# Performance work log

Hardware: AMD Instinct MI355X
Metric: run time of the kernel (lower is better)

The kernel has to match this reference:

```python
import jax, jax.numpy as jnp
import numpy as np

EPS = 1e-12

def l2norm(x, axis):
    # torch.nn.functional.normalize: x / max(||x||_2, eps)
    n = jnp.sqrt(jnp.sum(x * x, axis=axis, keepdims=True))
    return x / jnp.maximum(n, EPS)

def setup_inputs() -> dict:
    key = jax.random.key(0)
    k1, k2, k3, k4 = jax.random.split(key, 4)
    B, Cf, H, W = 128, 1024, 16, 16
    n_att, dv = 312, 300
    img = jax.random.normal(k1, (B, Cf, H, W), dtype=jnp.float32)
    # V is initialized from row-normalized w2v embeddings in the module
    V = l2norm(jax.random.normal(k2, (n_att, dv), dtype=jnp.float32), axis=1)
    W1 = jax.random.normal(k3, (dv, Cf), dtype=jnp.float32)
    W2 = jax.random.normal(k4, (dv, Cf), dtype=jnp.float32)
    return {"img": img, "V": V, "W1": W1, "W2": W2}

def reference(img, V, W1, W2):
    vv = l2norm(V, axis=1)                               # [i, v]
    B, Cf, H, Wd = img.shape
    av = l2norm(img.reshape(B, Cf, H * Wd), axis=1)      # [b, f, r]
    Q = vv @ W1                                          # [i, f]
    A = jnp.einsum('if,bfr->bir', Q, av)                 # attention logits
    A = jax.nn.softmax(A, axis=-1)
    F_p = jnp.einsum('bir,bfr->bif', A, av)              # attended features
    Pred_att = jnp.einsum('if,bif->bi', vv @ W2, F_p)
    return Pred_att
```

## Files before the change

kernel.cpp:

```cpp
#include <hip/hip_runtime.h>
#include <math.h>

#define NB   128
#define CF   1024
#define RR   256
#define NA   312
#define DV   300
#define M2   320
#define MT   640
#define NKC  32

typedef _Float16 half8  __attribute__((ext_vector_type(8)));
typedef float float16v  __attribute__((ext_vector_type(16)));

__device__ __forceinline__ void gload16(const void* g, void* l) {
    __builtin_amdgcn_global_load_lds(
        (const __attribute__((address_space(1))) void*)g,
        (__attribute__((address_space(3))) void*)l, 16, 0, 0);
}

__global__ void k_prep(const float* __restrict__ img, float* __restrict__ sumsq,
                       _Float16* __restrict__ avT) {
    int fs = blockIdx.x, rc = blockIdx.y, b = blockIdx.z;
    int r0 = rc * 64;
    int t = threadIdx.x;
    __shared__ __align__(16) char sm[64 * 65 * 4];
    _Float16 (*tile)[65] = (_Float16 (*)[65])sm;
    float    (*ssb)[65]  = (float    (*)[65])sm;
    int fl = t >> 2, cg = t & 3;
    int rl = t >> 2, g  = t & 3;
    float ss[16];
    #pragma unroll
    for (int j = 0; j < 16; ++j) ss[j] = 0.f;

    for (int fc = 0; fc < 4; ++fc) {
        int f0 = fs * 256 + fc * 64;
        const float4* p4 = (const float4*)(img + ((size_t)(b * CF + f0 + fl)) * RR + r0 + cg * 16);
        float4 v0 = p4[0], v1 = p4[1], v2 = p4[2], v3 = p4[3];
        __syncthreads();
        float xs[16] = {v0.x, v0.y, v0.z, v0.w, v1.x, v1.y, v1.z, v1.w,
                        v2.x, v2.y, v2.z, v2.w, v3.x, v3.y, v3.z, v3.w};
        #pragma unroll
        for (int j = 0; j < 16; ++j) {
            ss[j] += xs[j] * xs[j];
            tile[fl][cg * 16 + j] = (_Float16)xs[j];
        }
        __syncthreads();
        int kc  = (f0 >> 5) + (g >> 1);
        int kkb = (g & 1) * 16;
        half8 o0, o1;
        #pragma unroll
        for (int j = 0; j < 8; ++j) o0[j] = tile[g * 16 + j][rl];
        #pragma unroll
        for (int j = 0; j < 8; ++j) o1[j] = tile[g * 16 + 8 + j][rl];
        _Float16* q = avT + (((size_t)(b * NKC + kc) * RR + r0 + rl) * 32 + kkb);
        *(half8*)q       = o0;
        *(half8*)(q + 8) = o1;
    }
    __syncthreads();
    #pragma unroll
    for (int j = 0; j < 16; ++j) ssb[fl][cg * 16 + j] = ss[j];
    __syncthreads();
    if (t < 64) {
        float tot = 0.f;
        for (int f2 = 0; f2 < 64; ++f2) tot += ssb[f2][t];
        atomicAdd(&sumsq[b * RR + r0 + t], tot);
    }
}

__global__ void k_q(const float* __restrict__ V, const float* __restrict__ W1,
                    const float* __restrict__ W2, _Float16* __restrict__ Qb) {
    int ib = blockIdx.x;
    int f  = blockIdx.y * 256 + threadIdx.x;
    int i0 = ib * 8;
    int t  = threadIdx.x;
    __shared__ float inv8[8];
    float acc[8] = {0,0,0,0,0,0,0,0};
    bool zero = (ib == 39 || ib == 79);
    int v0 = (ib < 40) ? i0 : i0 - M2;
    if (!zero) {
        int row = t >> 5, l32 = t & 31;
        float s = 0.f;
        for (int v = l32; v < DV; v += 32) { float x = V[(v0 + row) * DV + v]; s += x * x; }
        #pragma unroll
        for (int o = 16; o; o >>= 1) s += __shfl_xor(s, o, 32);
        if (l32 == 0) inv8[row] = 1.f / fmaxf(sqrtf(s), 1e-12f);
        __syncthreads();
        const float* W = (ib < 40) ? W1 : W2;
        for (int v = 0; v < DV; ++v) {
            float wv = W[(size_t)v * CF + f];
            #pragma unroll
            for (int ii = 0; ii < 8; ++ii) acc[ii] += V[(v0 + ii) * DV + v] * wv;
        }
        #pragma unroll
        for (int ii = 0; ii < 8; ++ii) acc[ii] *= inv8[ii];
    }
    #pragma unroll
    for (int ii = 0; ii < 8; ++ii)
        Qb[((size_t)(f >> 5) * MT + (i0 + ii)) * 32 + (f & 31)] = (_Float16)acc[ii];
}

__launch_bounds__(256, 4)
__global__ void k_gemm(const _Float16* __restrict__ Qb, const _Float16* __restrict__ avT,
                       const float* __restrict__ sumsq, float* __restrict__ out) {
    int lin  = blockIdx.x;
    int xcd  = lin & 7;
    int slot = lin >> 3;
    int bq   = slot / 10;
    int t    = slot - bq * 10;
    int b    = bq * 8 + xcd;

    int tid = threadIdx.x;
    int lane = tid & 63, w = tid >> 6;
    int nl = lane & 31, kh = lane >> 5;

    __shared__ __align__(16) char smem[40960];
    _Float16* A0 = (_Float16*)smem;
    _Float16* A1 = (_Float16*)(smem + 4096);
    _Float16* B0 = (_Float16*)(smem + 8192);
    _Float16* B1 = (_Float16*)(smem + 24576);
    float* inv  = (float*)smem;
    float* mred = (float*)(smem + 1024);
    float* mg   = (float*)(smem + 1536);
    float* sred = (float*)(smem + 1664);
    float* dred = (float*)(smem + 2176);

    float16v acc[2][2];
    #pragma unroll
    for (int i = 0; i < 2; ++i)
        #pragma unroll
        for (int j = 0; j < 2; ++j)
            #pragma unroll
            for (int gidx = 0; gidx < 16; ++gidx) acc[i][j][gidx] = 0.f;

    int arow = (lane < 32) ? (t * 32 + lane) : (M2 + t * 32 + (lane - 32));
    int brow = w * 64 + lane;
    const _Float16* bpanel = avT + (size_t)b * NKC * RR * 32;

    #define STAGE(kc_, Adst, Bdst)                                              \
        do {                                                                    \
            const _Float16* abase = Qb + (size_t)(kc_) * MT * 32;               \
            gload16(abase + (size_t)arow * 32 + w * 8, (Adst) + w * 512);       \
            const _Float16* bbase = bpanel + (size_t)(kc_) * RR * 32;           \
            gload16(bbase + (size_t)brow * 32 + 0 * 8, (Bdst) + 0 * 2048 + w * 512); \
            gload16(bbase + (size_t)brow * 32 + 1 * 8, (Bdst) + 1 * 2048 + w * 512); \
            gload16(bbase + (size_t)brow * 32 + 2 * 8, (Bdst) + 2 * 2048 + w * 512); \
            gload16(bbase + (size_t)brow * 32 + 3 * 8, (Bdst) + 3 * 2048 + w * 512); \
        } while (0)

    #define COMPUTE(Al, Bl)                                                     \
        do {                                                                    \
            _Pragma("unroll")                                                   \
            for (int ks = 0; ks < 2; ++ks) {                                    \
                int kb = ks * 2 + kh;                                           \
                half8 a0 = *(const half8*)((Al) + (kb * 64 + nl) * 8);          \
                half8 a1 = *(const half8*)((Al) + (kb * 64 + 32 + nl) * 8);     \
                half8 b0 = *(const half8*)((Bl) + (kb * 256 + w * 64 + nl) * 8);\
                half8 b1 = *(const half8*)((Bl) + (kb * 256 + w * 64 + 32 + nl) * 8);\
                acc[0][0] = __builtin_amdgcn_mfma_f32_32x32x16_f16(a0, b0, acc[0][0], 0, 0, 0); \
                acc[0][1] = __builtin_amdgcn_mfma_f32_32x32x16_f16(a0, b1, acc[0][1], 0, 0, 0); \
                acc[1][0] = __builtin_amdgcn_mfma_f32_32x32x16_f16(a1, b0, acc[1][0], 0, 0, 0); \
                acc[1][1] = __builtin_amdgcn_mfma_f32_32x32x16_f16(a1, b1, acc[1][1], 0, 0, 0); \
            }                                                                   \
        } while (0)

    STAGE(0, A0, B0);

    for (int kc = 0; kc < NKC; kc += 2) {
        __syncthreads();
        STAGE(kc + 1, A1, B1);
        COMPUTE(A0, B0);
        __syncthreads();
        if (kc + 2 < NKC) STAGE(kc + 2, A0, B0);
        COMPUTE(A1, B1);
    }
    __syncthreads();

    inv[tid] = 1.f / fmaxf(sqrtf(sumsq[b * RR + tid]), 1e-12f);
    __syncthreads();

    float iv0 = inv[w * 64 + nl];
    float iv1 = inv[w * 64 + 32 + nl];
    #pragma unroll
    for (int gidx = 0; gidx < 16; ++gidx) {
        acc[0][0][gidx] *= iv0; acc[0][1][gidx] *= iv1;
        acc[1][0][gidx] *= iv0; acc[1][1][gidx] *= iv1;
    }
    float mx[16];
    #pragma unroll
    for (int gidx = 0; gidx < 16; ++gidx) mx[gidx] = fmaxf(acc[0][0][gidx], acc[0][1][gidx]);
    #pragma unroll
    for (int off = 1; off <= 16; off <<= 1)
        #pragma unroll
        for (int gidx = 0; gidx < 16; ++gidx)
            mx[gidx] = fmaxf(mx[gidx], __shfl_xor(mx[gidx], off, 64));
    if (nl == 0) {
        #pragma unroll
        for (int gidx = 0; gidx < 16; ++gidx) {
            int row = (gidx & 3) + 8 * (gidx >> 2) + 4 * kh;
            mred[row * 4 + w] = mx[gidx];
        }
    }
    __syncthreads();
    if (tid < 32)
        mg[tid] = fmaxf(fmaxf(mred[tid * 4], mred[tid * 4 + 1]),
                        fmaxf(mred[tid * 4 + 2], mred[tid * 4 + 3]));
    __syncthreads();
    float sp[16], dp[16];
    #pragma unroll
    for (int gidx = 0; gidx < 16; ++gidx) {
        int row = (gidx & 3) + 8 * (gidx >> 2) + 4 * kh;
        float m  = mg[row];
        float e0 = __expf(acc[0][0][gidx] - m);
        float e1 = __expf(acc[0][1][gidx] - m);
        sp[gidx] = e0 + e1;
        dp[gidx] = e0 * acc[1][0][gidx] + e1 * acc[1][1][gidx];
    }
    #pragma unroll
    for (int off = 1; off <= 16; off <<= 1)
        #pragma unroll
        for (int gidx = 0; gidx < 16; ++gidx) {
            sp[gidx] += __shfl_xor(sp[gidx], off, 64);
            dp[gidx] += __shfl_xor(dp[gidx], off, 64);
        }
    if (nl == 0) {
        #pragma unroll
        for (int gidx = 0; gidx < 16; ++gidx) {
            int row = (gidx & 3) + 8 * (gidx >> 2) + 4 * kh;
            sred[row * 4 + w] = sp[gidx];
            dred[row * 4 + w] = dp[gidx];
        }
    }
    __syncthreads();
    if (tid < 32) {
        float s = sred[tid * 4] + sred[tid * 4 + 1] + sred[tid * 4 + 2] + sred[tid * 4 + 3];
        float d = dred[tid * 4] + dred[tid * 4 + 1] + dred[tid * 4 + 2] + dred[tid * 4 + 3];
        int ig = t * 32 + tid;
        if (ig < NA) out[b * NA + ig] = d / s;
    }
    #undef STAGE
    #undef COMPUTE
}

extern "C" void kernel_launch(void* const* d_in, const int* in_sizes, int n_in,
                              void* d_out, int out_size, void* d_ws, size_t ws_size,
                              hipStream_t stream) {
    const float* img = (const float*)d_in[0];
    const float* V   = (const float*)d_in[1];
    const float* W1  = (const float*)d_in[2];
    const float* W2  = (const float*)d_in[3];
    float* out = (float*)d_out;

    char* ws = (char*)d_ws;
    size_t off = 0;
    float*    sumsq = (float*)(ws + off);    off += (size_t)NB * RR * 4;
    _Float16* avT   = (_Float16*)(ws + off); off += (size_t)NB * CF * RR * 2;
    _Float16* Qb    = (_Float16*)(ws + off); off += (size_t)NKC * MT * 32 * 2;

    hipMemsetAsync(sumsq, 0, (size_t)NB * RR * 4, stream);

    k_prep<<<dim3(4, 4, NB), 256, 0, stream>>>(img, sumsq, avT);
    k_q<<<dim3(80, 4), 256, 0, stream>>>(V, W1, W2, Qb);
    k_gemm<<<dim3(1280), 256, 0, stream>>>(Qb, avT, sumsq, out);
}
```

Measured before the change: 325.1 us.

## Load GEMM operands straight to registers, double the per-block tile, drop atomics

The GEMM kernel no longer stages A/B tiles through LDS with global_load_lds and barriers. Each wave now loads its half8 fragments directly from global memory into registers, double-buffered, and each block covers 64 attribute rows instead of 32, so it launches half as many blocks. The prep kernel loops over all 1024 channels per block, which lets it write the inverse norm directly and drops the memset, the atomics and the per-block sqrt in the GEMM. The risks are higher register pressure (launch bounds lowered to 2), redundant global loads of Qb and avT across waves without LDS sharing, and fewer prep blocks for the bandwidth-bound pass.

```diff
diff --git a/kernel.cpp b/kernel.cpp
--- a/kernel.cpp
+++ b/kernel.cpp
@@ -13,15 +13,9 @@
 typedef _Float16 half8  __attribute__((ext_vector_type(8)));
 typedef float float16v  __attribute__((ext_vector_type(16)));
 
-__device__ __forceinline__ void gload16(const void* g, void* l) {
-    __builtin_amdgcn_global_load_lds(
-        (const __attribute__((address_space(1))) void*)g,
-        (__attribute__((address_space(3))) void*)l, 16, 0, 0);
-}
-
-__global__ void k_prep(const float* __restrict__ img, float* __restrict__ sumsq,
+__global__ void k_prep(const float* __restrict__ img, float* __restrict__ invg,
                        _Float16* __restrict__ avT) {
-    int fs = blockIdx.x, rc = blockIdx.y, b = blockIdx.z;
+    int rc = blockIdx.x, b = blockIdx.y;
     int r0 = rc * 64;
     int t = threadIdx.x;
     __shared__ __align__(16) char sm[64 * 65 * 4];
@@ -33,8 +27,8 @@
     #pragma unroll
     for (int j = 0; j < 16; ++j) ss[j] = 0.f;
 
-    for (int fc = 0; fc < 4; ++fc) {
-        int f0 = fs * 256 + fc * 64;
+    for (int cc = 0; cc < 16; ++cc) {
+        int f0 = cc * 64;
         const float4* p4 = (const float4*)(img + ((size_t)(b * CF + f0 + fl)) * RR + r0 + cg * 16);
         float4 v0 = p4[0], v1 = p4[1], v2 = p4[2], v3 = p4[3];
         __syncthreads();
@@ -64,7 +58,7 @@
     if (t < 64) {
         float tot = 0.f;
         for (int f2 = 0; f2 < 64; ++f2) tot += ssb[f2][t];
-        atomicAdd(&sumsq[b * RR + r0 + t], tot);
+        invg[b * RR + r0 + t] = 1.f / fmaxf(sqrtf(tot), 1e-12f);
     }
 }
 
@@ -100,146 +94,152 @@
         Qb[((size_t)(f >> 5) * MT + (i0 + ii)) * 32 + (f & 31)] = (_Float16)acc[ii];
 }
 
-__launch_bounds__(256, 4)
+__launch_bounds__(256, 2)
 __global__ void k_gemm(const _Float16* __restrict__ Qb, const _Float16* __restrict__ avT,
-                       const float* __restrict__ sumsq, float* __restrict__ out) {
+                       const float* __restrict__ invg, float* __restrict__ out) {
     int lin  = blockIdx.x;
     int xcd  = lin & 7;
     int slot = lin >> 3;
-    int bq   = slot / 10;
-    int t    = slot - bq * 10;
+    int bq   = slot / 5;
+    int t2   = slot - bq * 5;
     int b    = bq * 8 + xcd;
 
     int tid = threadIdx.x;
     int lane = tid & 63, w = tid >> 6;
     int nl = lane & 31, kh = lane >> 5;
 
-    __shared__ __align__(16) char smem[40960];
-    _Float16* A0 = (_Float16*)smem;
-    _Float16* A1 = (_Float16*)(smem + 4096);
-    _Float16* B0 = (_Float16*)(smem + 8192);
-    _Float16* B1 = (_Float16*)(smem + 24576);
-    float* inv  = (float*)smem;
-    float* mred = (float*)(smem + 1024);
-    float* mg   = (float*)(smem + 1536);
-    float* sred = (float*)(smem + 1664);
-    float* dred = (float*)(smem + 2176);
-
-    float16v acc[2][2];
-    #pragma unroll
-    for (int i = 0; i < 2; ++i)
+    int rq1 = t2 * 64 + nl;
+    int rq2 = M2 + t2 * 64 + nl;
+    int cB  = w * 64 + nl;
+
+    __shared__ float mred[64 * 4];
+    __shared__ float mg[64];
+    __shared__ float sred[64 * 4];
+    __shared__ float dred[64 * 4];
+
+    float16v acc[4][2];
+    #pragma unroll
+    for (int i = 0; i < 4; ++i)
         #pragma unroll
         for (int j = 0; j < 2; ++j)
             #pragma unroll
-            for (int gidx = 0; gidx < 16; ++gidx) acc[i][j][gidx] = 0.f;
-
-    int arow = (lane < 32) ? (t * 32 + lane) : (M2 + t * 32 + (lane - 32));
-    int brow = w * 64 + lane;
-    const _Float16* bpanel = avT + (size_t)b * NKC * RR * 32;
-
-    #define STAGE(kc_, Adst, Bdst)                                              \
-        do {                                                                    \
-            const _Float16* abase = Qb + (size_t)(kc_) * MT * 32;               \
-            gload16(abase + (size_t)arow * 32 + w * 8, (Adst) + w * 512);       \
-            const _Float16* bbase = bpanel + (size_t)(kc_) * RR * 32;           \
-            gload16(bbase + (size_t)brow * 32 + 0 * 8, (Bdst) + 0 * 2048 + w * 512); \
-            gload16(bbase + (size_t)brow * 32 + 1 * 8, (Bdst) + 1 * 2048 + w * 512); \
-            gload16(bbase + (size_t)brow * 32 + 2 * 8, (Bdst) + 2 * 2048 + w * 512); \
-            gload16(bbase + (size_t)brow * 32 + 3 * 8, (Bdst) + 3 * 2048 + w * 512); \
-        } while (0)
-
-    #define COMPUTE(Al, Bl)                                                     \
-        do {                                                                    \
-            _Pragma("unroll")                                                   \
-            for (int ks = 0; ks < 2; ++ks) {                                    \
-                int kb = ks * 2 + kh;                                           \
-                half8 a0 = *(const half8*)((Al) + (kb * 64 + nl) * 8);          \
-                half8 a1 = *(const half8*)((Al) + (kb * 64 + 32 + nl) * 8);     \
-                half8 b0 = *(const half8*)((Bl) + (kb * 256 + w * 64 + nl) * 8);\
-                half8 b1 = *(const half8*)((Bl) + (kb * 256 + w * 64 + 32 + nl) * 8);\
-                acc[0][0] = __builtin_amdgcn_mfma_f32_32x32x16_f16(a0, b0, acc[0][0], 0, 0, 0); \
-                acc[0][1] = __builtin_amdgcn_mfma_f32_32x32x16_f16(a0, b1, acc[0][1], 0, 0, 0); \
-                acc[1][0] = __builtin_amdgcn_mfma_f32_32x32x16_f16(a1, b0, acc[1][0], 0, 0, 0); \
-                acc[1][1] = __builtin_amdgcn_mfma_f32_32x32x16_f16(a1, b1, acc[1][1], 0, 0, 0); \
-            }                                                                   \
-        } while (0)
-
-    STAGE(0, A0, B0);
-
+            for (int gi = 0; gi < 16; ++gi) acc[i][j][gi] = 0.f;
+
+    half8 aA[8], bA[4], aB[8], bB[4];
+
+    #define LOADF(Aa, Bb, kc_) do {                                              \
+        const _Float16* ab = Qb + (size_t)(kc_) * MT * 32 + kh * 8;              \
+        Aa[0] = *(const half8*)(ab + (size_t)rq1 * 32);                          \
+        Aa[1] = *(const half8*)(ab + (size_t)rq1 * 32 + 16);                     \
+        Aa[2] = *(const half8*)(ab + (size_t)rq2 * 32);                          \
+        Aa[3] = *(const half8*)(ab + (size_t)rq2 * 32 + 16);                     \
+        Aa[4] = *(const half8*)(ab + (size_t)(rq1 + 32) * 32);                   \
+        Aa[5] = *(const half8*)(ab + (size_t)(rq1 + 32) * 32 + 16);              \
+        Aa[6] = *(const half8*)(ab + (size_t)(rq2 + 32) * 32);                   \
+        Aa[7] = *(const half8*)(ab + (size_t)(rq2 + 32) * 32 + 16);              \
+        const _Float16* bb = avT + ((size_t)(b * NKC + (kc_)) * RR + cB) * 32 + kh * 8; \
+        Bb[0] = *(const half8*)(bb);                                             \
+        Bb[1] = *(const half8*)(bb + 16);                                        \
+        Bb[2] = *(const half8*)(bb + 32 * 32);                                   \
+        Bb[3] = *(const half8*)(bb + 32 * 32 + 16);                              \
+    } while (0)
+
+    #define COMP(Aa, Bb) do {                                                    \
+        _Pragma("unroll")                                                        \
+        for (int ks = 0; ks < 2; ++ks)                                           \
+            _Pragma("unroll")                                                    \
+            for (int rf = 0; rf < 4; ++rf)                                       \
+                _Pragma("unroll")                                                \
+                for (int cb = 0; cb < 2; ++cb)                                   \
+                    acc[rf][cb] = __builtin_amdgcn_mfma_f32_32x32x16_f16(        \
+                        Aa[rf * 2 + ks], Bb[cb * 2 + ks], acc[rf][cb], 0, 0, 0); \
+    } while (0)
+
+    LOADF(aA, bA, 0);
     for (int kc = 0; kc < NKC; kc += 2) {
-        __syncthreads();
-        STAGE(kc + 1, A1, B1);
-        COMPUTE(A0, B0);
-        __syncthreads();
-        if (kc + 2 < NKC) STAGE(kc + 2, A0, B0);
-        COMPUTE(A1, B1);
-    }
-    __syncthreads();
-
-    inv[tid] = 1.f / fmaxf(sqrtf(sumsq[b * RR + tid]), 1e-12f);
-    __syncthreads();
-
-    float iv0 = inv[w * 64 + nl];
-    float iv1 = inv[w * 64 + 32 + nl];
-    #pragma unroll
-    for (int gidx = 0; gidx < 16; ++gidx) {
-        acc[0][0][gidx] *= iv0; acc[0][1][gidx] *= iv1;
-        acc[1][0][gidx] *= iv0; acc[1][1][gidx] *= iv1;
-    }
-    float mx[16];
-    #pragma unroll
-    for (int gidx = 0; gidx < 16; ++gidx) mx[gidx] = fmaxf(acc[0][0][gidx], acc[0][1][gidx]);
+        LOADF(aB, bB, kc + 1);
+        COMP(aA, bA);
+        if (kc + 2 < NKC) LOADF(aA, bA, kc + 2);
+        COMP(aB, bB);
+    }
+    #undef LOADF
+    #undef COMP
+
+    float iv0 = invg[b * RR + w * 64 + nl];
+    float iv1 = invg[b * RR + w * 64 + 32 + nl];
+    #pragma unroll
+    for (int rf = 0; rf < 4; ++rf)
+        #pragma unroll
+        for (int gi = 0; gi < 16; ++gi) {
+            acc[rf][0][gi] *= iv0;
+            acc[rf][1][gi] *= iv1;
+        }
+
+    float mx[2][16];
+    #pragma unroll
+    for (int p = 0; p < 2; ++p)
+        #pragma unroll
+        for (int gi = 0; gi < 16; ++gi)
+            mx[p][gi] = fmaxf(acc[2 * p][0][gi], acc[2 * p][1][gi]);
     #pragma unroll
     for (int off = 1; off <= 16; off <<= 1)
         #pragma unroll
-        for (int gidx = 0; gidx < 16; ++gidx)
-            mx[gidx] = fmaxf(mx[gidx], __shfl_xor(mx[gidx], off, 64));
+        for (int p = 0; p < 2; ++p)
+            #pragma unroll
+            for (int gi = 0; gi < 16; ++gi)
+                mx[p][gi] = fmaxf(mx[p][gi], __shfl_xor(mx[p][gi], off, 64));
     if (nl == 0) {
         #pragma unroll
-        for (int gidx = 0; gidx < 16; ++gidx) {
-            int row = (gidx & 3) + 8 * (gidx >> 2) + 4 * kh;
-            mred[row * 4 + w] = mx[gidx];
-        }
-    }
-    __syncthreads();
-    if (tid < 32)
+        for (int p = 0; p < 2; ++p)
+            #pragma unroll
+            for (int gi = 0; gi < 16; ++gi) {
+                int row = (gi & 3) + 8 * (gi >> 2) + 4 * kh;
+                mred[(p * 32 + row) * 4 + w] = mx[p][gi];
+            }
+    }
+    __syncthreads();
+    if (tid < 64)
         mg[tid] = fmaxf(fmaxf(mred[tid * 4], mred[tid * 4 + 1]),
                         fmaxf(mred[tid * 4 + 2], mred[tid * 4 + 3]));
     __syncthreads();
-    float sp[16], dp[16];
-    #pragma unroll
-    for (int gidx = 0; gidx < 16; ++gidx) {
-        int row = (gidx & 3) + 8 * (gidx >> 2) + 4 * kh;
-        float m  = mg[row];
-        float e0 = __expf(acc[0][0][gidx] - m);
-        float e1 = __expf(acc[0][1][gidx] - m);
-        sp[gidx] = e0 + e1;
-        dp[gidx] = e0 * acc[1][0][gidx] + e1 * acc[1][1][gidx];
-    }
+    float sp[2][16], dp[2][16];
+    #pragma unroll
+    for (int p = 0; p < 2; ++p)
+        #pragma unroll
+        for (int gi = 0; gi < 16; ++gi) {
+            int row = (gi & 3) + 8 * (gi >> 2) + 4 * kh;
+            float m  = mg[p * 32 + row];
+            float e0 = __expf(acc[2 * p][0][gi] - m);
+            float e1 = __expf(acc[2 * p][1][gi] - m);
+            sp[p][gi] = e0 + e1;
+            dp[p][gi] = e0 * acc[2 * p + 1][0][gi] + e1 * acc[2 * p + 1][1][gi];
+        }
     #pragma unroll
     for (int off = 1; off <= 16; off <<= 1)
         #pragma unroll
-        for (int gidx = 0; gidx < 16; ++gidx) {
-            sp[gidx] += __shfl_xor(sp[gidx], off, 64);
-            dp[gidx] += __shfl_xor(dp[gidx], off, 64);
-        }
+        for (int p = 0; p < 2; ++p)
+            #pragma unroll
+            for (int gi = 0; gi < 16; ++gi) {
+                sp[p][gi] += __shfl_xor(sp[p][gi], off, 64);
+                dp[p][gi] += __shfl_xor(dp[p][gi], off, 64);
+            }
     if (nl == 0) {
         #pragma unroll
-        for (int gidx = 0; gidx < 16; ++gidx) {
-            int row = (gidx & 3) + 8 * (gidx >> 2) + 4 * kh;
-            sred[row * 4 + w] = sp[gidx];
-            dred[row * 4 + w] = dp[gidx];
-        }
-    }
-    __syncthreads();
-    if (tid < 32) {
+        for (int p = 0; p < 2; ++p)
+            #pragma unroll
+            for (int gi = 0; gi < 16; ++gi) {
+                int row = (gi & 3) + 8 * (gi >> 2) + 4 * kh;
+                sred[(p * 32 + row) * 4 + w] = sp[p][gi];
+                dred[(p * 32 + row) * 4 + w] = dp[p][gi];
+            }
+    }
+    __syncthreads();
+    if (tid < 64) {
         float s = sred[tid * 4] + sred[tid * 4 + 1] + sred[tid * 4 + 2] + sred[tid * 4 + 3];
         float d = dred[tid * 4] + dred[tid * 4 + 1] + dred[tid * 4 + 2] + dred[tid * 4 + 3];
-        int ig = t * 32 + tid;
+        int ig = t2 * 64 + tid;
         if (ig < NA) out[b * NA + ig] = d / s;
     }
-    #undef STAGE
-    #undef COMPUTE
 }
 
 extern "C" void kernel_launch(void* const* d_in, const int* in_sizes, int n_in,
@@ -253,13 +253,11 @@
 
     char* ws = (char*)d_ws;
     size_t off = 0;
-    float*    sumsq = (float*)(ws + off);    off += (size_t)NB * RR * 4;
-    _Float16* avT   = (_Float16*)(ws + off); off += (size_t)NB * CF * RR * 2;
-    _Float16* Qb    = (_Float16*)(ws + off); off += (size_t)NKC * MT * 32 * 2;
-
-    hipMemsetAsync(sumsq, 0, (size_t)NB * RR * 4, stream);
-
-    k_prep<<<dim3(4, 4, NB), 256, 0, stream>>>(img, sumsq, avT);
+    float*    invg = (float*)(ws + off);    off += (size_t)NB * RR * 4;
+    _Float16* avT  = (_Float16*)(ws + off); off += (size_t)NB * CF * RR * 2;
+    _Float16* Qb   = (_Float16*)(ws + off); off += (size_t)NKC * MT * 32 * 2;
+
+    k_prep<<<dim3(4, NB), 256, 0, stream>>>(img, invg, avT);
     k_q<<<dim3(80, 4), 256, 0, stream>>>(V, W1, W2, Qb);
-    k_gemm<<<dim3(1280), 256, 0, stream>>>(Qb, avT, sumsq, out);
-}
+    k_gemm<<<dim3(640), 256, 0, stream>>>(Qb, avT, invg, out);
+}
```

After: 329.9 us. No clear change (+1.5%).
